# Optimization experiments

Measured on AMD Instinct MI355X. Metric: run time of the kernel, lower is better.

Reference implementation:

```python
import jax, jax.numpy as jnp
import numpy as np

B, T, D, H = 16, 1024, 768, 64

def setup_inputs() -> dict:
    key = jax.random.key(0)
    k1, k2, k3, k4 = jax.random.split(key, 4)
    scale = 0.02
    x = jax.random.normal(k1, (B, T, D), dtype=jnp.float32)
    Wq = jax.random.normal(k2, (H, D), dtype=jnp.float32) * scale
    Wk = jax.random.normal(k3, (H, D), dtype=jnp.float32) * scale
    Wv = jax.random.normal(k4, (H, D), dtype=jnp.float32) * scale
    return {"x": x, "Wq": Wq, "Wk": Wk, "Wv": Wv}

def reference(x, Wq, Wk, Wv):
    # q,k,v: [B,T,H]  (nn.Linear with no bias: x @ W^T)
    q = jnp.einsum('btd,hd->bth', x, Wq)
    k = jnp.einsum('btd,hd->bth', x, Wk)
    v = jnp.einsum('btd,hd->bth', x, Wv)
    T_ = x.shape[1]
    # NOTE: original scales by emb_dim**-0.5 (not head_size**-0.5)
    scores = jnp.einsum('bth,bsh->bts', q, k) * (x.shape[-1] ** -0.5)
    causal = jnp.tril(jnp.ones((T_, T_), dtype=bool))
    scores = jnp.where(causal, scores, -jnp.inf)
    attn = jax.nn.softmax(scores, axis=-1)
    return jnp.einsum('bts,bsh->bth', attn, v)
```

## Files before the change

### kernel.cpp

```cpp
#include <hip/hip_runtime.h>
#include <hip/hip_bf16.h>

typedef __attribute__((ext_vector_type(8))) short bf16x8;
typedef __attribute__((ext_vector_type(4))) float f32x4;

#define BATCH 16
#define SEQ   1024
#define EMB   768
#define HEAD  64
#define NT    (BATCH*SEQ)
#define NQKV  192
#define OSTR  104

__device__ inline ushort f2bf(float f) {
  __hip_bfloat16 h = __float2bfloat16(f);
  return *reinterpret_cast<const ushort*>(&h);
}

__device__ inline void lds_dma16(const void* g, void* l) {
  __builtin_amdgcn_global_load_lds(
      (const __attribute__((address_space(1))) void*)g,
      (__attribute__((address_space(3))) void*)l, 16, 0, 0);
}

__global__ __launch_bounds__(256) void conv_kernel(
    const float* __restrict__ x, const float* __restrict__ Wq,
    const float* __restrict__ Wk, const float* __restrict__ Wv,
    ushort* __restrict__ xbf, ushort* __restrict__ wt)
{
  if (blockIdx.x < 2048) {
    const int row = blockIdx.x * 8 + (threadIdx.x >> 5);
    #pragma unroll
    for (int j = 0; j < 3; ++j) {
      const int c = (threadIdx.x & 31) + 32 * j;
      const int grp = c >> 3, gst = c & 7;
      const int glog = gst ^ (row & 7);
      const int srccol = (grp << 6) + (glog << 3);
      const float4 f0 = *reinterpret_cast<const float4*>(&x[(size_t)row * EMB + srccol]);
      const float4 f1 = *reinterpret_cast<const float4*>(&x[(size_t)row * EMB + srccol + 4]);
      union { ushort us[8]; uint4 u; } o;
      o.us[0]=f2bf(f0.x); o.us[1]=f2bf(f0.y); o.us[2]=f2bf(f0.z); o.us[3]=f2bf(f0.w);
      o.us[4]=f2bf(f1.x); o.us[5]=f2bf(f1.y); o.us[6]=f2bf(f1.z); o.us[7]=f2bf(f1.w);
      *reinterpret_cast<uint4*>(&xbf[(size_t)row * EMB + (c << 3)]) = o.u;
    }
  } else {
    const int row = (blockIdx.x - 2048) * 8 + (threadIdx.x >> 5);
    const float* W = (row < 64) ? Wq : (row < 128 ? Wk : Wv);
    const int r = row & 63;
    #pragma unroll
    for (int j = 0; j < 3; ++j) {
      const int c = (threadIdx.x & 31) + 32 * j;
      const int grp = c >> 3, gst = c & 7;
      const int glog = gst ^ (row & 7);
      const int srccol = (grp << 6) + (glog << 3);
      const float4 f0 = *reinterpret_cast<const float4*>(&W[(size_t)r * EMB + srccol]);
      const float4 f1 = *reinterpret_cast<const float4*>(&W[(size_t)r * EMB + srccol + 4]);
      union { ushort us[8]; uint4 u; } o;
      o.us[0]=f2bf(f0.x); o.us[1]=f2bf(f0.y); o.us[2]=f2bf(f0.z); o.us[3]=f2bf(f0.w);
      o.us[4]=f2bf(f1.x); o.us[5]=f2bf(f1.y); o.us[6]=f2bf(f1.z); o.us[7]=f2bf(f1.w);
      *reinterpret_cast<uint4*>(&wt[(size_t)row * EMB + (c << 3)]) = o.u;
    }
  }
}

__global__ __launch_bounds__(256) void proj_kernel(
    const ushort* __restrict__ xbf, const ushort* __restrict__ wt,
    ushort* __restrict__ qo, ushort* __restrict__ ko, ushort* __restrict__ vo)
{
  __shared__ ushort Xl[2][32 * 64];
  __shared__ ushort Wl[2][96 * 64];

  const int tid  = threadIdx.x;
  const int wave = tid >> 6, lane = tid & 63;
  const int mb   = blockIdx.x >> 1, nb = blockIdx.x & 1;
  const int m0   = mb * 32;
  const int nb96 = nb * 96;
  const int wr   = wave >> 1, wc = wave & 1;
  const int col16 = lane & 15, quad = lane >> 4;

  #define STAGE(kt_, buf_) { _Pragma("unroll")                                  \
    for (int u5 = 0; u5 < 4; ++u5) {                                            \
      const int u = wave * 4 + u5;                                              \
      if (u < 4) {                                                              \
        lds_dma16(&xbf[(size_t)(m0 + u * 8 + (lane >> 3)) * EMB + (kt_) * 64 + (lane & 7) * 8], \
                  &Xl[buf_][u * 512]);                                          \
      } else {                                                                  \
        const int s = u - 4;                                                    \
        lds_dma16(&wt[(size_t)(nb96 + s * 8 + (lane >> 3)) * EMB + (kt_) * 64 + (lane & 7) * 8], \
                  &Wl[buf_][s * 512]);                                          \
      } } }

  f32x4 acc[3];
  #pragma unroll
  for (int n = 0; n < 3; ++n) acc[n] = (f32x4){0.f, 0.f, 0.f, 0.f};

  STAGE(0, 0);

  for (int kt = 0; kt < 12; ++kt) {
    const int cur = kt & 1;
    __syncthreads();
    if (kt < 11) STAGE(kt + 1, cur ^ 1);
    #pragma unroll
    for (int ks = 0; ks < 2; ++ks) {
      const int g = ks * 4 + quad;
      const int ar = wr * 16 + col16;
      const bf16x8 a = *reinterpret_cast<const bf16x8*>(
          &Xl[cur][ar * 64 + ((g ^ (ar & 7)) << 3)]);
      #pragma unroll
      for (int n = 0; n < 3; ++n) {
        const int br = wc * 48 + 16 * n + col16;
        const bf16x8 b = *reinterpret_cast<const bf16x8*>(
            &Wl[cur][br * 64 + ((g ^ (br & 7)) << 3)]);
        acc[n] = __builtin_amdgcn_mfma_f32_16x16x32_bf16(a, b, acc[n], 0, 0, 0);
      }
    }
  }

  __syncthreads();
  {
    ushort* RP = &Wl[0][0];
    const int tr = wr * 16 + quad * 4;
    #pragma unroll
    for (int n = 0; n < 3; ++n)
      #pragma unroll
      for (int i = 0; i < 4; ++i)
        RP[(tr + i) * OSTR + wc * 48 + n * 16 + col16] = f2bf(acc[n][i]);
    __syncthreads();

    if (nb == 0) {
      {
        const int rr = tid >> 3, g = tid & 7;
        *reinterpret_cast<uint4*>(&qo[(size_t)(m0 + rr) * HEAD + g * 8]) =
            *reinterpret_cast<const uint4*>(&RP[rr * OSTR + g * 8]);
      }
      if (tid < 128) {
        const int rr = tid >> 2, lg = tid & 3;
        const int c = lg ^ (rr & 7);
        *reinterpret_cast<uint4*>(&ko[(size_t)(m0 + rr) * HEAD + c * 8]) =
            *reinterpret_cast<const uint4*>(&RP[rr * OSTR + 64 + lg * 8]);
      }
    } else {
      if (tid < 128) {
        const int rr = tid >> 2, l4 = tid & 3;
        const int lg = 4 + l4;
        const int c = lg ^ (rr & 7);
        *reinterpret_cast<uint4*>(&ko[(size_t)(m0 + rr) * HEAD + c * 8]) =
            *reinterpret_cast<const uint4*>(&RP[rr * OSTR + l4 * 8]);
      }
      {
        const int h = tid >> 2, d = tid & 3;
        const int w = (m0 & 63) >> 3;
        const int lg = w + d;
        const int c = lg ^ (h & 7);
        union { ushort us[8]; uint4 u; } pv;
        #pragma unroll
        for (int e = 0; e < 8; ++e)
          pv.us[e] = RP[(d * 8 + e) * OSTR + 32 + h];
        const int bb = m0 >> 10;
        const int tb64 = (m0 & 1023) & ~63;
        *reinterpret_cast<uint4*>(
            &vo[((size_t)bb * HEAD + h) * SEQ + tb64 + c * 8]) = pv.u;
      }
    }
  }
  #undef STAGE
}

__global__ __launch_bounds__(256) void attn_kernel(
    const ushort* __restrict__ q, const ushort* __restrict__ k,
    const ushort* __restrict__ vT, float* __restrict__ out,
    float* __restrict__ po, float* __restrict__ pl)
{
  __shared__ ushort Kl[2][64 * 64];
  __shared__ ushort Vl[2][64 * 64];
  __shared__ ushort lp[4][16][72];

  const int tid  = threadIdx.x;
  const int wave = tid >> 6, lane = tid & 63;
  const int bid  = blockIdx.x;
  const int b    = bid & 15;
  const int u    = bid >> 4;

  int j, s, ns;
  if (u < 4)       { j = u;                s = 0;           ns = 1; }
  else if (u < 12) { j = 4 + ((u - 4) >> 1);  s = (u - 4) & 1; ns = 2; }
  else             { j = 8 + ((u - 12) >> 2); s = (u - 12) & 3; ns = 4; }

  const int qt0 = j * 64;
  const int nt  = j + 1;
  const int t0  = (nt * s) / ns;
  const int t1  = (nt * (s + 1)) / ns;
  const float SC2 = 0.03608439182435161f * 1.4426950408889634f;

  const int col  = lane & 15;
  const int quad = lane >> 4;
  const int koff = quad * 8;

  const size_t qb = ((size_t)b * SEQ + qt0 + 16 * wave + col) * HEAD;
  const bf16x8 qa0 = *reinterpret_cast<const bf16x8*>(&q[qb + koff]);
  const bf16x8 qa1 = *reinterpret_cast<const bf16x8*>(&q[qb + koff + 32]);

  #define STAGE(t_, buf_) {                                                     \
    _Pragma("unroll")                                                           \
    for (int r = 0; r < 2; ++r)                                                 \
      lds_dma16(&k[((size_t)b * SEQ + (t_) * 64 + r * 32 + wave * 8 + (lane >> 3)) * HEAD + (lane & 7) * 8], \
                &Kl[buf_][(r * 32 + wave * 8) * 64]);                           \
    _Pragma("unroll")                                                           \
    for (int r = 0; r < 2; ++r)                                                 \
      lds_dma16(&vT[((size_t)b * HEAD + r * 32 + wave * 8 + (lane >> 3)) * SEQ + (t_) * 64 + (lane & 7) * 8], \
                &Vl[buf_][(r * 32 + wave * 8) * 64]);                           \
  }

  f32x4 o[4];
  #pragma unroll
  for (int hf = 0; hf < 4; ++hf) o[hf] = (f32x4){0.f, 0.f, 0.f, 0.f};
  float l_part[4];
  #pragma unroll
  for (int i = 0; i < 4; ++i) l_part[i] = 0.f;

  STAGE(t0, 0);

  for (int t = t0; t < t1; ++t) {
    const int cur = (t - t0) & 1;
    __syncthreads();
    if (t + 1 < t1) STAGE(t + 1, cur ^ 1);

    f32x4 sreg[4];
    #pragma unroll
    for (int f = 0; f < 4; ++f) {
      const int rowf = 16 * f + col;
      const bf16x8 kb0 = *reinterpret_cast<const bf16x8*>(
          &Kl[cur][rowf * 64 + ((quad ^ (rowf & 7)) << 3)]);
      const bf16x8 kb1 = *reinterpret_cast<const bf16x8*>(
          &Kl[cur][rowf * 64 + (((quad + 4) ^ (rowf & 7)) << 3)]);
      f32x4 z = (f32x4){0.f, 0.f, 0.f, 0.f};
      z       = __builtin_amdgcn_mfma_f32_16x16x32_bf16(qa0, kb0, z, 0, 0, 0);
      sreg[f] = __builtin_amdgcn_mfma_f32_16x16x32_bf16(qa1, kb1, z, 0, 0, 0);
    }

    const bool last = (t == nt - 1);
    #pragma unroll
    for (int f = 0; f < 4; ++f) {
      const int kvc = t * 64 + 16 * f + col;
      #pragma unroll
      for (int i = 0; i < 4; ++i) {
        float v = sreg[f][i];
        if (last && kvc > qt0 + 16 * wave + quad * 4 + i) v = -1e30f;
        const float p = exp2f(v * SC2);
        l_part[i] += p;
        lp[wave][quad * 4 + i][16 * f + col] = f2bf(p);
      }
    }

    #pragma unroll
    for (int ks = 0; ks < 2; ++ks) {
      const bf16x8 pa = *reinterpret_cast<const bf16x8*>(&lp[wave][col][ks * 32 + koff]);
      #pragma unroll
      for (int hf = 0; hf < 4; ++hf) {
        const int vrow = 16 * hf + col;
        const int g = ks * 4 + quad;
        const bf16x8 vb = *reinterpret_cast<const bf16x8*>(
            &Vl[cur][vrow * 64 + ((g ^ (vrow & 7)) << 3)]);
        o[hf] = __builtin_amdgcn_mfma_f32_16x16x32_bf16(pa, vb, o[hf], 0, 0, 0);
      }
    }
  }

  #pragma unroll
  for (int i = 0; i < 4; ++i) {
    #pragma unroll
    for (int d = 1; d < 16; d <<= 1) l_part[i] += __shfl_xor(l_part[i], d);
  }

  if (ns == 1) {
    #pragma unroll
    for (int i = 0; i < 4; ++i) {
      const float inv = 1.0f / l_part[i];
      const int tq = qt0 + 16 * wave + quad * 4 + i;
      #pragma unroll
      for (int hf = 0; hf < 4; ++hf)
        out[((size_t)b * SEQ + tq) * HEAD + 16 * hf + col] = o[hf][i] * inv;
    }
  } else {
    const int su = u - 4;
    const int pidx = b * 40 + su;
    float* pob = &po[(size_t)pidx * 4096];
    #pragma unroll
    for (int i = 0; i < 4; ++i) {
      const int r = 16 * wave + quad * 4 + i;
      #pragma unroll
      for (int hf = 0; hf < 4; ++hf)
        pob[r * 64 + 16 * hf + col] = o[hf][i];
      if (col == 0) pl[pidx * 64 + r] = l_part[i];
    }
  }
  #undef STAGE
}

__global__ __launch_bounds__(256) void combine_kernel(
    const float* __restrict__ po, const float* __restrict__ pl,
    float* __restrict__ out)
{
  const int idx = blockIdx.x * 256 + threadIdx.x;
  const int c = idx & 63;
  const int r = (idx >> 6) & 63;
  const int e = idx >> 12;
  const int jj = e % 12, b = e / 12;
  const int j = 4 + jj;
  const int su0 = (j < 8) ? (j - 4) * 2 : 8 + (j - 8) * 4;
  const int ns  = (j < 8) ? 2 : 4;
  float num = 0.f, den = 0.f;
  for (int s = 0; s < ns; ++s) {
    const int pidx = b * 40 + su0 + s;
    num += po[(size_t)pidx * 4096 + r * 64 + c];
    den += pl[pidx * 64 + r];
  }
  out[((size_t)b * SEQ + j * 64 + r) * HEAD + c] = num / den;
}

extern "C" void kernel_launch(void* const* d_in, const int* in_sizes, int n_in,
                              void* d_out, int out_size, void* d_ws, size_t ws_size,
                              hipStream_t stream) {
  const float* x  = (const float*)d_in[0];
  const float* Wq = (const float*)d_in[1];
  const float* Wk = (const float*)d_in[2];
  const float* Wv = (const float*)d_in[3];

  char* base = (char*)d_ws;
  ushort* qw  = (ushort*)(base);
  ushort* kw  = (ushort*)(base + (2u << 20));
  ushort* vTw = (ushort*)(base + (4u << 20));
  ushort* wtw = (ushort*)(base + (6u << 20));
  ushort* xbf = (ushort*)(base + (7u << 20));
  float*  po  = (float*) (base + (32u << 20));
  float*  pl  = (float*) (base + (44u << 20));
  float*  out = (float*)d_out;

  conv_kernel<<<2048 + NQKV / 8, 256, 0, stream>>>(x, Wq, Wk, Wv, xbf, wtw);
  proj_kernel<<<(NT / 32) * 2, 256, 0, stream>>>(xbf, wtw, qw, kw, vTw);
  attn_kernel<<<BATCH * 44, 256, 0, stream>>>(qw, kw, vTw, out, po, pl);
  combine_kernel<<<786432 / 256, 256, 0, stream>>>(po, pl, out);
}
```

Before: 45.49 us.

## Double projection M-tile to 64 rows per block for weight reuse

The projection kernel now handles 64 token rows per block instead of 32. Each wave computes a 2x3 grid of MFMA tiles, so every loaded weight fragment is reused across two A fragments, and the weight tile is loaded from global memory half as often in total. The grid halves to 512 blocks and the V-transpose epilogue is rewritten for full 64-token chunks. The cost is more registers and LDS per block and fewer blocks to hide latency; the launch bound adds a minimum-occupancy hint.

```diff
diff --git a/kernel.cpp b/kernel.cpp
--- a/kernel.cpp
+++ b/kernel.cpp
@@ -63,36 +63,40 @@
   }
 }
 
-__global__ __launch_bounds__(256) void proj_kernel(
+__global__ __launch_bounds__(256, 4) void proj_kernel(
     const ushort* __restrict__ xbf, const ushort* __restrict__ wt,
     ushort* __restrict__ qo, ushort* __restrict__ ko, ushort* __restrict__ vo)
 {
-  __shared__ ushort Xl[2][32 * 64];
+  __shared__ ushort Xl[2][64 * 64];
   __shared__ ushort Wl[2][96 * 64];
 
   const int tid  = threadIdx.x;
   const int wave = tid >> 6, lane = tid & 63;
   const int mb   = blockIdx.x >> 1, nb = blockIdx.x & 1;
-  const int m0   = mb * 32;
+  const int m0   = mb * 64;
   const int nb96 = nb * 96;
   const int wr   = wave >> 1, wc = wave & 1;
   const int col16 = lane & 15, quad = lane >> 4;
 
-  #define STAGE(kt_, buf_) { _Pragma("unroll")                                  \
-    for (int u5 = 0; u5 < 4; ++u5) {                                            \
-      const int u = wave * 4 + u5;                                              \
-      if (u < 4) {                                                              \
-        lds_dma16(&xbf[(size_t)(m0 + u * 8 + (lane >> 3)) * EMB + (kt_) * 64 + (lane & 7) * 8], \
-                  &Xl[buf_][u * 512]);                                          \
-      } else {                                                                  \
-        const int s = u - 4;                                                    \
-        lds_dma16(&wt[(size_t)(nb96 + s * 8 + (lane >> 3)) * EMB + (kt_) * 64 + (lane & 7) * 8], \
-                  &Wl[buf_][s * 512]);                                          \
-      } } }
-
-  f32x4 acc[3];
+  #define STAGE(kt_, buf_) {                                                    \
+    _Pragma("unroll")                                                           \
+    for (int e = 0; e < 2; ++e) {                                               \
+      const int u = wave * 2 + e;                                               \
+      lds_dma16(&xbf[(size_t)(m0 + u * 8 + (lane >> 3)) * EMB + (kt_) * 64 + (lane & 7) * 8], \
+                &Xl[buf_][u * 512]);                                            \
+    }                                                                           \
+    _Pragma("unroll")                                                           \
+    for (int e = 0; e < 3; ++e) {                                               \
+      const int s = wave * 3 + e;                                               \
+      lds_dma16(&wt[(size_t)(nb96 + s * 8 + (lane >> 3)) * EMB + (kt_) * 64 + (lane & 7) * 8], \
+                &Wl[buf_][s * 512]);                                            \
+    } }
+
+  f32x4 acc[2][3];
   #pragma unroll
-  for (int n = 0; n < 3; ++n) acc[n] = (f32x4){0.f, 0.f, 0.f, 0.f};
+  for (int m = 0; m < 2; ++m)
+    #pragma unroll
+    for (int n = 0; n < 3; ++n) acc[m][n] = (f32x4){0.f, 0.f, 0.f, 0.f};
 
   STAGE(0, 0);
 
@@ -103,15 +107,21 @@
     #pragma unroll
     for (int ks = 0; ks < 2; ++ks) {
       const int g = ks * 4 + quad;
-      const int ar = wr * 16 + col16;
-      const bf16x8 a = *reinterpret_cast<const bf16x8*>(
-          &Xl[cur][ar * 64 + ((g ^ (ar & 7)) << 3)]);
+      bf16x8 a[2];
+      #pragma unroll
+      for (int m = 0; m < 2; ++m) {
+        const int ar = wr * 32 + 16 * m + col16;
+        a[m] = *reinterpret_cast<const bf16x8*>(
+            &Xl[cur][ar * 64 + ((g ^ (ar & 7)) << 3)]);
+      }
       #pragma unroll
       for (int n = 0; n < 3; ++n) {
         const int br = wc * 48 + 16 * n + col16;
         const bf16x8 b = *reinterpret_cast<const bf16x8*>(
             &Wl[cur][br * 64 + ((g ^ (br & 7)) << 3)]);
-        acc[n] = __builtin_amdgcn_mfma_f32_16x16x32_bf16(a, b, acc[n], 0, 0, 0);
+        #pragma unroll
+        for (int m = 0; m < 2; ++m)
+          acc[m][n] = __builtin_amdgcn_mfma_f32_16x16x32_bf16(a[m], b, acc[m][n], 0, 0, 0);
       }
     }
   }
@@ -119,28 +129,32 @@
   __syncthreads();
   {
     ushort* RP = &Wl[0][0];
-    const int tr = wr * 16 + quad * 4;
-    #pragma unroll
-    for (int n = 0; n < 3; ++n)
-      #pragma unroll
-      for (int i = 0; i < 4; ++i)
-        RP[(tr + i) * OSTR + wc * 48 + n * 16 + col16] = f2bf(acc[n][i]);
+    #pragma unroll
+    for (int m = 0; m < 2; ++m)
+      #pragma unroll
+      for (int n = 0; n < 3; ++n)
+        #pragma unroll
+        for (int i = 0; i < 4; ++i)
+          RP[(wr * 32 + 16 * m + quad * 4 + i) * OSTR + wc * 48 + n * 16 + col16]
+              = f2bf(acc[m][n][i]);
     __syncthreads();
 
     if (nb == 0) {
-      {
-        const int rr = tid >> 3, g = tid & 7;
+      #pragma unroll
+      for (int e = 0; e < 2; ++e) {
+        const int slot = tid + 256 * e;
+        const int rr = slot >> 3, g = slot & 7;
         *reinterpret_cast<uint4*>(&qo[(size_t)(m0 + rr) * HEAD + g * 8]) =
             *reinterpret_cast<const uint4*>(&RP[rr * OSTR + g * 8]);
       }
-      if (tid < 128) {
+      {
         const int rr = tid >> 2, lg = tid & 3;
         const int c = lg ^ (rr & 7);
         *reinterpret_cast<uint4*>(&ko[(size_t)(m0 + rr) * HEAD + c * 8]) =
             *reinterpret_cast<const uint4*>(&RP[rr * OSTR + 64 + lg * 8]);
       }
     } else {
-      if (tid < 128) {
+      {
         const int rr = tid >> 2, l4 = tid & 3;
         const int lg = 4 + l4;
         const int c = lg ^ (rr & 7);
@@ -148,18 +162,19 @@
             *reinterpret_cast<const uint4*>(&RP[rr * OSTR + l4 * 8]);
       }
       {
-        const int h = tid >> 2, d = tid & 3;
-        const int w = (m0 & 63) >> 3;
-        const int lg = w + d;
-        const int c = lg ^ (h & 7);
-        union { ushort us[8]; uint4 u; } pv;
+        const int bb = m0 >> 10, tb = m0 & 1023;
         #pragma unroll
-        for (int e = 0; e < 8; ++e)
-          pv.us[e] = RP[(d * 8 + e) * OSTR + 32 + h];
-        const int bb = m0 >> 10;
-        const int tb64 = (m0 & 1023) & ~63;
-        *reinterpret_cast<uint4*>(
-            &vo[((size_t)bb * HEAD + h) * SEQ + tb64 + c * 8]) = pv.u;
+        for (int e = 0; e < 2; ++e) {
+          const int slot = tid + 256 * e;
+          const int h = slot >> 3, d = slot & 7;
+          const int c = d ^ (h & 7);
+          union { ushort us[8]; uint4 u; } pv;
+          #pragma unroll
+          for (int ee = 0; ee < 8; ++ee)
+            pv.us[ee] = RP[(d * 8 + ee) * OSTR + 32 + h];
+          *reinterpret_cast<uint4*>(
+              &vo[((size_t)bb * HEAD + h) * SEQ + tb + c * 8]) = pv.u;
+        }
       }
     }
   }
@@ -337,7 +352,7 @@
   float*  out = (float*)d_out;
 
   conv_kernel<<<2048 + NQKV / 8, 256, 0, stream>>>(x, Wq, Wk, Wv, xbf, wtw);
-  proj_kernel<<<(NT / 32) * 2, 256, 0, stream>>>(xbf, wtw, qw, kw, vTw);
+  proj_kernel<<<(NT / 64) * 2, 256, 0, stream>>>(xbf, wtw, qw, kw, vTw);
   attn_kernel<<<BATCH * 44, 256, 0, stream>>>(qw, kw, vTw, out, po, pl);
   combine_kernel<<<786432 / 256, 256, 0, stream>>>(po, pl, out);
 }
```

Measured after the change: 49.14 us. 1.08x slower.

## Fuse x fp32-to-bf16 conversion into projection kernel staging

Applied to the files above, without the earlier changes.

Drops the separate pass that converted all of x to bf16 in global memory. The projection kernel now loads fp32 x tiles into registers, converts them, and writes them swizzled into LDS after the MFMA work of each step. Weights still go through DMA to LDS. This removes the intermediate bf16 write and read and one launch. In exchange, each x tile is read in fp32 by both column-half blocks, and the x staging moves from async DMA to register loads.

```diff
diff --git a/kernel.cpp b/kernel.cpp
--- a/kernel.cpp
+++ b/kernel.cpp
@@ -23,48 +23,30 @@
       (__attribute__((address_space(3))) void*)l, 16, 0, 0);
 }
 
-__global__ __launch_bounds__(256) void conv_kernel(
-    const float* __restrict__ x, const float* __restrict__ Wq,
-    const float* __restrict__ Wk, const float* __restrict__ Wv,
-    ushort* __restrict__ xbf, ushort* __restrict__ wt)
+__global__ __launch_bounds__(256) void convw_kernel(
+    const float* __restrict__ Wq, const float* __restrict__ Wk,
+    const float* __restrict__ Wv, ushort* __restrict__ wt)
 {
-  if (blockIdx.x < 2048) {
-    const int row = blockIdx.x * 8 + (threadIdx.x >> 5);
-    #pragma unroll
-    for (int j = 0; j < 3; ++j) {
-      const int c = (threadIdx.x & 31) + 32 * j;
-      const int grp = c >> 3, gst = c & 7;
-      const int glog = gst ^ (row & 7);
-      const int srccol = (grp << 6) + (glog << 3);
-      const float4 f0 = *reinterpret_cast<const float4*>(&x[(size_t)row * EMB + srccol]);
-      const float4 f1 = *reinterpret_cast<const float4*>(&x[(size_t)row * EMB + srccol + 4]);
-      union { ushort us[8]; uint4 u; } o;
-      o.us[0]=f2bf(f0.x); o.us[1]=f2bf(f0.y); o.us[2]=f2bf(f0.z); o.us[3]=f2bf(f0.w);
-      o.us[4]=f2bf(f1.x); o.us[5]=f2bf(f1.y); o.us[6]=f2bf(f1.z); o.us[7]=f2bf(f1.w);
-      *reinterpret_cast<uint4*>(&xbf[(size_t)row * EMB + (c << 3)]) = o.u;
-    }
-  } else {
-    const int row = (blockIdx.x - 2048) * 8 + (threadIdx.x >> 5);
-    const float* W = (row < 64) ? Wq : (row < 128 ? Wk : Wv);
-    const int r = row & 63;
-    #pragma unroll
-    for (int j = 0; j < 3; ++j) {
-      const int c = (threadIdx.x & 31) + 32 * j;
-      const int grp = c >> 3, gst = c & 7;
-      const int glog = gst ^ (row & 7);
-      const int srccol = (grp << 6) + (glog << 3);
-      const float4 f0 = *reinterpret_cast<const float4*>(&W[(size_t)r * EMB + srccol]);
-      const float4 f1 = *reinterpret_cast<const float4*>(&W[(size_t)r * EMB + srccol + 4]);
-      union { ushort us[8]; uint4 u; } o;
-      o.us[0]=f2bf(f0.x); o.us[1]=f2bf(f0.y); o.us[2]=f2bf(f0.z); o.us[3]=f2bf(f0.w);
-      o.us[4]=f2bf(f1.x); o.us[5]=f2bf(f1.y); o.us[6]=f2bf(f1.z); o.us[7]=f2bf(f1.w);
-      *reinterpret_cast<uint4*>(&wt[(size_t)row * EMB + (c << 3)]) = o.u;
-    }
+  const int row = blockIdx.x * 8 + (threadIdx.x >> 5);
+  const float* W = (row < 64) ? Wq : (row < 128 ? Wk : Wv);
+  const int r = row & 63;
+  #pragma unroll
+  for (int j = 0; j < 3; ++j) {
+    const int c = (threadIdx.x & 31) + 32 * j;
+    const int grp = c >> 3, gst = c & 7;
+    const int glog = gst ^ (row & 7);
+    const int srccol = (grp << 6) + (glog << 3);
+    const float4 f0 = *reinterpret_cast<const float4*>(&W[(size_t)r * EMB + srccol]);
+    const float4 f1 = *reinterpret_cast<const float4*>(&W[(size_t)r * EMB + srccol + 4]);
+    union { ushort us[8]; uint4 u; } o;
+    o.us[0]=f2bf(f0.x); o.us[1]=f2bf(f0.y); o.us[2]=f2bf(f0.z); o.us[3]=f2bf(f0.w);
+    o.us[4]=f2bf(f1.x); o.us[5]=f2bf(f1.y); o.us[6]=f2bf(f1.z); o.us[7]=f2bf(f1.w);
+    *reinterpret_cast<uint4*>(&wt[(size_t)row * EMB + (c << 3)]) = o.u;
   }
 }
 
 __global__ __launch_bounds__(256) void proj_kernel(
-    const ushort* __restrict__ xbf, const ushort* __restrict__ wt,
+    const float* __restrict__ x, const ushort* __restrict__ wt,
     ushort* __restrict__ qo, ushort* __restrict__ ko, ushort* __restrict__ vo)
 {
   __shared__ ushort Xl[2][32 * 64];
@@ -78,28 +60,38 @@
   const int wr   = wave >> 1, wc = wave & 1;
   const int col16 = lane & 15, quad = lane >> 4;
 
-  #define STAGE(kt_, buf_) { _Pragma("unroll")                                  \
-    for (int u5 = 0; u5 < 4; ++u5) {                                            \
-      const int u = wave * 4 + u5;                                              \
-      if (u < 4) {                                                              \
-        lds_dma16(&xbf[(size_t)(m0 + u * 8 + (lane >> 3)) * EMB + (kt_) * 64 + (lane & 7) * 8], \
-                  &Xl[buf_][u * 512]);                                          \
-      } else {                                                                  \
-        const int s = u - 4;                                                    \
-        lds_dma16(&wt[(size_t)(nb96 + s * 8 + (lane >> 3)) * EMB + (kt_) * 64 + (lane & 7) * 8], \
-                  &Wl[buf_][s * 512]);                                          \
-      } } }
+  const int xrow = tid >> 3;
+  const int xchk = tid & 7;
+
+  float4 xa, xb;
+
+  #define LOADX(kt_) {                                                          \
+    const float* p = &x[(size_t)(m0 + xrow) * EMB + (kt_) * 64 + xchk * 8];     \
+    xa = *reinterpret_cast<const float4*>(p);                                   \
+    xb = *reinterpret_cast<const float4*>(p + 4); }
+
+  #define WRITEX(buf_) {                                                        \
+    union { ushort us[8]; uint4 u; } p;                                         \
+    p.us[0]=f2bf(xa.x); p.us[1]=f2bf(xa.y); p.us[2]=f2bf(xa.z); p.us[3]=f2bf(xa.w); \
+    p.us[4]=f2bf(xb.x); p.us[5]=f2bf(xb.y); p.us[6]=f2bf(xb.z); p.us[7]=f2bf(xb.w); \
+    *reinterpret_cast<uint4*>(&Xl[buf_][xrow * 64 + ((xchk ^ (xrow & 7)) << 3)]) = p.u; }
+
+  #define STAGEW(kt_, buf_) { _Pragma("unroll")                                 \
+    for (int u = 0; u < 3; ++u) {                                               \
+      lds_dma16(&wt[(size_t)(nb96 + u * 32 + wave * 8 + (lane >> 3)) * EMB + (kt_) * 64 + (lane & 7) * 8], \
+                &Wl[buf_][(u * 32 + wave * 8) * 64]);                           \
+    } }
 
   f32x4 acc[3];
   #pragma unroll
   for (int n = 0; n < 3; ++n) acc[n] = (f32x4){0.f, 0.f, 0.f, 0.f};
 
-  STAGE(0, 0);
-
+  LOADX(0); STAGEW(0, 0); WRITEX(0);
+
+  int cur = 0;
   for (int kt = 0; kt < 12; ++kt) {
-    const int cur = kt & 1;
     __syncthreads();
-    if (kt < 11) STAGE(kt + 1, cur ^ 1);
+    if (kt < 11) { LOADX(kt + 1); STAGEW(kt + 1, cur ^ 1); }
     #pragma unroll
     for (int ks = 0; ks < 2; ++ks) {
       const int g = ks * 4 + quad;
@@ -114,6 +106,8 @@
         acc[n] = __builtin_amdgcn_mfma_f32_16x16x32_bf16(a, b, acc[n], 0, 0, 0);
       }
     }
+    if (kt < 11) WRITEX(cur ^ 1);
+    cur ^= 1;
   }
 
   __syncthreads();
@@ -163,7 +157,9 @@
       }
     }
   }
-  #undef STAGE
+  #undef LOADX
+  #undef WRITEX
+  #undef STAGEW
 }
 
 __global__ __launch_bounds__(256) void attn_kernel(
@@ -331,13 +327,12 @@
   ushort* kw  = (ushort*)(base + (2u << 20));
   ushort* vTw = (ushort*)(base + (4u << 20));
   ushort* wtw = (ushort*)(base + (6u << 20));
-  ushort* xbf = (ushort*)(base + (7u << 20));
-  float*  po  = (float*) (base + (32u << 20));
-  float*  pl  = (float*) (base + (44u << 20));
+  float*  po  = (float*) (base + (8u << 20));
+  float*  pl  = (float*) (base + (20u << 20));
   float*  out = (float*)d_out;
 
-  conv_kernel<<<2048 + NQKV / 8, 256, 0, stream>>>(x, Wq, Wk, Wv, xbf, wtw);
-  proj_kernel<<<(NT / 32) * 2, 256, 0, stream>>>(xbf, wtw, qw, kw, vTw);
+  convw_kernel<<<NQKV / 8, 256, 0, stream>>>(Wq, Wk, Wv, wtw);
+  proj_kernel<<<(NT / 32) * 2, 256, 0, stream>>>(x, wtw, qw, kw, vTw);
   attn_kernel<<<BATCH * 44, 256, 0, stream>>>(qw, kw, vTw, out, po, pl);
   combine_kernel<<<786432 / 256, 256, 0, stream>>>(po, pl, out);
 }
```

Result: no change. 45.31 us (-0.4%).
